# Performance work log

Measured on AMD Instinct MI355X. Metric: run time of the kernel, lower is better.

The kernel has to match this reference:

```python
import jax, jax.numpy as jnp
import numpy as np
from jax import lax

B, CIN, T = 16, 2, 4096
DM, DI, DS, DR, DC, NL = 128, 256, 16, 8, 4, 6  # d_model, d_inner, d_state, dt_rank, d_conv, n_layers


def setup_inputs():
    ks = iter(jax.random.split(jax.random.key(0), 48))
    def rn(shape, s=0.05):
        return jax.random.normal(next(ks), shape, jnp.float32) * s
    rng = np.random.default_rng(0)
    n_mask = int(round(0.25 / 0.02))
    starts = rng.choice(np.linspace(0.0, 1.0, int(round(1 / 0.02)), endpoint=False), n_mask, replace=False)
    m = np.ones((B, CIN, T), np.float32)
    for s0 in starts:
        m[:, :, int(T * s0):int(T * (s0 + 0.02))] = 0.0
    return {
        'x': jax.random.normal(next(ks), (B, CIN, T), jnp.float32),
        'mask': jnp.asarray(m),
        'enc_W0': rn((32, CIN, 3), 0.3), 'enc_b0': jnp.zeros(32), 'enc_g0': jnp.ones(32), 'enc_be0': jnp.zeros(32),
        'enc_W1': rn((64, 32, 3), 0.1), 'enc_b1': jnp.zeros(64), 'enc_g1': jnp.ones(64), 'enc_be1': jnp.zeros(64),
        'enc_W2': rn((128, 64, 3), 0.08), 'enc_b2': jnp.zeros(128), 'enc_g2': jnp.ones(128), 'enc_be2': jnp.zeros(128),
        'ln_g': jnp.ones((NL, DM)), 'ln_b': jnp.zeros((NL, DM)),
        'in_W': rn((NL, 2 * DI, DM)), 'conv_W': rn((NL, DI, DC), 0.3), 'conv_b': jnp.zeros((NL, DI)),
        'xp_W': rn((NL, DR + 2 * DS, DI)), 'dt_W': rn((NL, DI, DR), 0.2),
        'dt_b': jnp.full((NL, DI), -4.6, jnp.float32),  # softplus -> dt ~ 0.01
        'A_log': jnp.tile(jnp.log(jnp.arange(1, DS + 1, dtype=jnp.float32)), (NL, DI, 1)),
        'D_p': jnp.ones((NL, DI)), 'out_W': rn((NL, DM, DI)),
        'nf_g': jnp.ones(DM), 'nf_b': jnp.zeros(DM),
        'dec_W0': rn((128, 64, 3), 0.08), 'dec_b0': jnp.zeros(64), 'dec_g0': jnp.ones(64), 'dec_be0': jnp.zeros(64),
        'dec_W1': rn((64, 32, 3), 0.1), 'dec_b1': jnp.zeros(32), 'dec_g1': jnp.ones(32), 'dec_be1': jnp.zeros(32),
        'dec_W2': rn((32, CIN, 3), 0.1), 'dec_b2': jnp.zeros(CIN),
    }


def _conv(x, W, b, stride, pad):
    y = lax.conv_general_dilated(x, W, (stride,), [(pad, pad)], dimension_numbers=('NCH', 'OIH', 'NCH'))
    return y + b[None, :, None]


def _deconv(x, W, b, stride=2, pad=1, out_pad=1):
    # torch ConvTranspose1d weight (in, out, k) -> flipped conv with lhs dilation
    k = W.shape[-1]
    Wc = jnp.flip(W, -1).transpose(1, 0, 2)
    y = lax.conv_general_dilated(x, Wc, (1,), [(k - 1 - pad, k - 1 - pad + out_pad)],
                                 lhs_dilation=(stride,), dimension_numbers=('NCH', 'OIH', 'NCH'))
    return y + b[None, :, None]


def _gn1(x, g, b, eps=1e-5):  # GroupNorm(1, C) over (C, L)
    m = x.mean((1, 2), keepdims=True)
    v = ((x - m) ** 2).mean((1, 2), keepdims=True)
    return (x - m) * lax.rsqrt(v + eps) * g[None, :, None] + b[None, :, None]


def _ln(x, g, b, eps=1e-5):
    m = x.mean(-1, keepdims=True)
    v = ((x - m) ** 2).mean(-1, keepdims=True)
    return (x - m) * lax.rsqrt(v + eps) * g + b


def _mamba(u, in_W, conv_W, conv_b, xp_W, dt_W, dt_b, A_log, D_p, out_W):
    # u: (B, L, DM)
    xz = jnp.einsum('bld,ed->ble', u, in_W)            # (B, L, 2*DI)
    xi, z = xz[..., :DI], xz[..., DI:]
    xc = jnp.pad(xi.transpose(0, 2, 1), ((0, 0), (0, 0), (DC - 1, 0)))  # causal pad
    xc = lax.conv_general_dilated(xc, conv_W[:, None, :], (1,), [(0, 0)],
                                  feature_group_count=DI, dimension_numbers=('NCH', 'OIH', 'NCH'))
    xc = jax.nn.silu(xc + conv_b[None, :, None]).transpose(0, 2, 1)     # (B, L, DI)
    dbl = jnp.einsum('bld,ed->ble', xc, xp_W)          # (B, L, DR+2*DS)
    dt = jax.nn.softplus(jnp.einsum('blr,dr->bld', dbl[..., :DR], dt_W) + dt_b)
    Bm = dbl[..., DR:DR + DS]
    Cm = dbl[..., DR + DS:]
    A = -jnp.exp(A_log)                                # (DI, DS)
    dA = jnp.exp(dt[..., None] * A)                    # (B, L, DI, DS)
    dBx = dt[..., None] * Bm[:, :, None, :] * xc[..., None]
    def comb(e1, e2):
        a1, b1 = e1
        a2, b2 = e2
        return a1 * a2, a2 * b1 + b2
    _, h = lax.associative_scan(comb, (dA, dBx), axis=1)  # selective scan over L
    y = jnp.einsum('blds,bls->bld', h, Cm) + D_p * xc
    y = y * jax.nn.silu(z)
    return jnp.einsum('bld,ed->ble', y, out_W)          # (B, L, DM)


def _forward(x, mask, enc_W0, enc_b0, enc_g0, enc_be0, enc_W1, enc_b1, enc_g1, enc_be1,
             enc_W2, enc_b2, enc_g2, enc_be2, ln_g, ln_b, in_W, conv_W, conv_b, xp_W,
             dt_W, dt_b, A_log, D_p, out_W, nf_g, nf_b,
             dec_W0, dec_b0, dec_g0, dec_be0, dec_W1, dec_b1, dec_g1, dec_be1, dec_W2, dec_b2):
    gelu = lambda t: jax.nn.gelu(t, approximate=False)
    h = mask * x
    h = gelu(_gn1(_conv(h, enc_W0, enc_b0, 2, 1), enc_g0, enc_be0))
    h = gelu(_gn1(_conv(h, enc_W1, enc_b1, 2, 1), enc_g1, enc_be1))
    h = gelu(_gn1(_conv(h, enc_W2, enc_b2, 2, 1), enc_g2, enc_be2))
    s = h.transpose(0, 2, 1)                            # (B, L=T/8, DM)
    for i in range(NL):
        s = s + _mamba(_ln(s, ln_g[i], ln_b[i]), in_W[i], conv_W[i], conv_b[i],
                       xp_W[i], dt_W[i], dt_b[i], A_log[i], D_p[i], out_W[i])
    s = _ln(s, nf_g, nf_b)
    d = s.transpose(0, 2, 1)
    d = gelu(_gn1(_deconv(d, dec_W0, dec_b0), dec_g0, dec_be0))
    d = gelu(_gn1(_deconv(d, dec_W1, dec_b1), dec_g1, dec_be1))
    d = _deconv(d, dec_W2, dec_b2)                      # (B, CIN, T), no norm/act on last block
    return d


def reference(x, mask, enc_W0, enc_b0, enc_g0, enc_be0, enc_W1, enc_b1, enc_g1, enc_be1,
              enc_W2, enc_b2, enc_g2, enc_be2, ln_g, ln_b, in_W, conv_W, conv_b, xp_W,
              dt_W, dt_b, A_log, D_p, out_W, nf_g, nf_b,
              dec_W0, dec_b0, dec_g0, dec_be0, dec_W1, dec_b1, dec_g1, dec_be1, dec_W2, dec_b2):
    d = _forward(x, mask, enc_W0, enc_b0, enc_g0, enc_be0, enc_W1, enc_b1, enc_g1, enc_be1,
                 enc_W2, enc_b2, enc_g2, enc_be2, ln_g, ln_b, in_W, conv_W, conv_b, xp_W,
                 dt_W, dt_b, A_log, D_p, out_W, nf_g, nf_b,
                 dec_W0, dec_b0, dec_g0, dec_be0, dec_W1, dec_b1, dec_g1, dec_be1, dec_W2, dec_b2)
    return (d, x, mask)
```

## Files before the change

### kernel.cpp

```cpp
#include <hip/hip_runtime.h>
#include <hip/hip_bf16.h>
#include <math.h>

#define NB 16
#define TT 4096
#define LL 512
#define DM 128
#define DI 256
#define NLAYER 6
#define CL 32
#define NCH 16

typedef __bf16 bf16x8 __attribute__((ext_vector_type(8)));
typedef float f32x4 __attribute__((ext_vector_type(4)));
typedef unsigned short ushort;

static __device__ __forceinline__ float gelu_f(float v){
  return 0.5f*v*(1.f + erff(v*0.70710678118654752f));
}
static __device__ __forceinline__ float silu_f(float v){
  return v/(1.f + __expf(-v));
}
static __device__ __forceinline__ ushort f2b(float v){
  __hip_bfloat16 h = __float2bfloat16(v);
  return *(ushort*)&h;
}

__global__ __launch_bounds__(256) void k_maskmul(const float* __restrict__ x, const float* __restrict__ m,
                          float* __restrict__ out, int n){
  int i = blockIdx.x*256 + threadIdx.x;
  if (i < n) out[i] = x[i]*m[i];
}

__global__ __launch_bounds__(256) void k_castb(const float* __restrict__ in, ushort* __restrict__ out, int n){
  int i = blockIdx.x*256 + threadIdx.x;
  if (i < n) out[i] = f2b(in[i]);
}

__global__ __launch_bounds__(256) void k_trw(const float* __restrict__ in, float* __restrict__ out, int Ci, int Co){
  int idx = blockIdx.x*256 + threadIdx.x;
  int n = Ci*Co*3;
  if (idx >= n) return;
  int k = idx % 3;
  int o = (idx/3) % Co;
  int ci = idx/(3*Co);
  out[((size_t)o*Ci + ci)*3 + k] = in[idx];
}

template<int Ci, int Co, int TW, int OS>
__global__ __launch_bounds__(256) void k_conv_lds(const float* __restrict__ x, const float* __restrict__ W,
                        const float* __restrict__ bias, float* __restrict__ y, int Li){
  const int Lc = TW;
  const int Lo = Li >> 1;
  const int S  = Lo / Lc;
  const int CoB = Co / OS;
  __shared__ float xe[Ci][Lc+1];
  __shared__ float xo[Ci][Lc+1];
  int bid = blockIdx.x;
  int os = bid % OS;
  int ch = (bid / OS) % S;
  int b  = bid / (OS*S);
  int t0 = ch*Lc;
  const float* xb = x + (size_t)b*Ci*Li;
  for (int idx = threadIdx.x; idx < Ci*(2*Lc+1); idx += 256){
    int ci = idx / (2*Lc+1);
    int j  = idx - ci*(2*Lc+1);
    int gin = 2*t0 - 1 + j;
    float v = (gin >= 0 && gin < Li) ? xb[(size_t)ci*Li + gin] : 0.f;
    if (j & 1) xo[ci][j>>1] = v;
    else       xe[ci][j>>1] = v;
  }
  __syncthreads();
  const int NOg = 256/TW;
  const int OI  = CoB/NOg;
  int tl = threadIdx.x % TW;
  int og = threadIdx.x / TW;
  #pragma unroll
  for (int oi = 0; oi < OI; oi++){
    int o = os*CoB + oi*NOg + og;
    const float* w = W + (size_t)o*Ci*3;
    float acc = bias[o];
    #pragma unroll 4
    for (int ci = 0; ci < Ci; ci++){
      float w0 = w[ci*3+0], w1 = w[ci*3+1], w2 = w[ci*3+2];
      acc += w0*xe[ci][tl] + w1*xo[ci][tl] + w2*xe[ci][tl+1];
    }
    y[((size_t)b*Co + o)*Lo + t0 + tl] = acc;
  }
}

__global__ __launch_bounds__(256) void k_gn_part(const float* __restrict__ x, float* __restrict__ gp){
  int b = blockIdx.x >> 3, k8 = blockIdx.x & 7;
  const float* xb = x + (size_t)b*65536 + (size_t)k8*8192;
  float s = 0.f, s2 = 0.f;
  for (int i = threadIdx.x; i < 8192; i += 256){ float v = xb[i]; s += v; s2 += v*v; }
  #pragma unroll
  for (int o = 32; o; o >>= 1){ s += __shfl_down(s, o); s2 += __shfl_down(s2, o); }
  __shared__ float sh[8];
  int wid = threadIdx.x >> 6;
  if ((threadIdx.x & 63) == 0){ sh[wid] = s; sh[wid+4] = s2; }
  __syncthreads();
  if (threadIdx.x == 0){
    float a = sh[0]+sh[1]+sh[2]+sh[3], a2 = sh[4]+sh[5]+sh[6]+sh[7];
    gp[(b*8+k8)*2+0] = a; gp[(b*8+k8)*2+1] = a2;
  }
}
__global__ __launch_bounds__(256) void k_gn_apply(float* __restrict__ x, const float* __restrict__ g,
                          const float* __restrict__ be, int Tl, const float* __restrict__ gp){
  int gidx = blockIdx.x*256 + threadIdx.x;
  int b = gidx >> 16, i = gidx & 65535;
  float s = 0.f, s2 = 0.f;
  #pragma unroll
  for (int k = 0; k < 8; k++){ s += gp[(b*8+k)*2]; s2 += gp[(b*8+k)*2+1]; }
  float mean = s*(1.f/65536.f);
  float inv  = rsqrtf(s2*(1.f/65536.f) - mean*mean + 1e-5f);
  int c = i / Tl;
  float* p = x + (size_t)b*65536 + i;
  float v = (*p - mean)*inv*g[c] + be[c];
  *p = gelu_f(v);
}

__global__ __launch_bounds__(256) void k_transpose2(const float* __restrict__ in, float* __restrict__ out){
  int idx = blockIdx.x*256 + threadIdx.x;
  if (idx >= NB*DM*LL) return;
  int t = idx & 511;
  int c = (idx >> 9) & 127;
  int b = idx >> 16;
  out[(size_t)b*65536 + (size_t)t*128 + c] = in[idx];
}

__global__ __launch_bounds__(256) void k_transposeB(const float* __restrict__ in, float* __restrict__ out){
  int idx = blockIdx.x*256 + threadIdx.x;
  if (idx >= NB*DM*LL) return;
  int m = idx & 511;
  int c = (idx >> 9) & 127;
  int b = idx >> 16;
  out[idx] = in[(size_t)b*65536 + (size_t)m*128 + c];
}

__global__ __launch_bounds__(256) void k_ln2(const float* __restrict__ x, const float* __restrict__ g,
                      const float* __restrict__ be, float* __restrict__ out, int rows){
  int row = blockIdx.x*4 + (threadIdx.x >> 6);
  if (row >= rows) return;
  int lid = threadIdx.x & 63;
  const float* xr = x + (size_t)row*DM;
  float v0 = xr[lid], v1 = xr[lid+64];
  float s = v0 + v1;
  #pragma unroll
  for (int o = 32; o; o >>= 1) s += __shfl_xor(s, o);
  float mean = s*(1.f/128.f);
  float d0 = v0-mean, d1 = v1-mean;
  float s2 = d0*d0 + d1*d1;
  #pragma unroll
  for (int o = 32; o; o >>= 1) s2 += __shfl_xor(s2, o);
  float inv = rsqrtf(s2*(1.f/128.f) + 1e-5f);
  float* orow = out + (size_t)row*DM;
  orow[lid]    = d0*inv*g[lid]    + be[lid];
  orow[lid+64] = d1*inv*g[lid+64] + be[lid+64];
}

__global__ __launch_bounds__(256) void k_ln2b(const float* __restrict__ x, const float* __restrict__ g,
                      const float* __restrict__ be, ushort* __restrict__ out, int rows){
  int row = blockIdx.x*4 + (threadIdx.x >> 6);
  if (row >= rows) return;
  int lid = threadIdx.x & 63;
  const float* xr = x + (size_t)row*DM;
  float v0 = xr[lid], v1 = xr[lid+64];
  float s = v0 + v1;
  #pragma unroll
  for (int o = 32; o; o >>= 1) s += __shfl_xor(s, o);
  float mean = s*(1.f/128.f);
  float d0 = v0-mean, d1 = v1-mean;
  float s2 = d0*d0 + d1*d1;
  #pragma unroll
  for (int o = 32; o; o >>= 1) s2 += __shfl_xor(s2, o);
  float inv = rsqrtf(s2*(1.f/128.f) + 1e-5f);
  ushort* orow = out + (size_t)row*DM;
  orow[lid]    = f2b(d0*inv*g[lid]    + be[lid]);
  orow[lid+64] = f2b(d1*inv*g[lid+64] + be[lid+64]);
}

__global__ __launch_bounds__(256) void k_mfma_split(const ushort* __restrict__ A, const ushort* __restrict__ B,
                          float* __restrict__ C0, float* __restrict__ C1, int K){
  int tid = threadIdx.x;
  int wid = tid >> 6, l = tid & 63;
  int wm = wid >> 1, wn = wid & 1;
  int m0 = blockIdx.y*128 + wm*64;
  int n0 = blockIdx.x*128 + wn*64;
  int lr = l & 15;
  int lk = (l >> 4)*8;
  int orow = (l >> 4)*4;
  f32x4 acc[4][4];
  #pragma unroll
  for (int i = 0; i < 4; i++)
    #pragma unroll
    for (int j = 0; j < 4; j++) acc[i][j] = (f32x4){0.f,0.f,0.f,0.f};
  for (int k0 = 0; k0 < K; k0 += 32){
    bf16x8 a[4], b[4];
    #pragma unroll
    for (int f = 0; f < 4; f++)
      a[f] = *(const bf16x8*)(A + (size_t)(m0 + f*16 + lr)*K + k0 + lk);
    #pragma unroll
    for (int f = 0; f < 4; f++)
      b[f] = *(const bf16x8*)(B + (size_t)(n0 + f*16 + lr)*K + k0 + lk);
    #pragma unroll
    for (int i = 0; i < 4; i++)
      #pragma unroll
      for (int j = 0; j < 4; j++)
        acc[i][j] = __builtin_amdgcn_mfma_f32_16x16x32_bf16(a[i], b[j], acc[i][j], 0, 0, 0);
  }
  float* C    = (n0 < 256) ? C0 : C1;
  int ncol0   = (n0 < 256) ? n0 : n0 - 256;
  #pragma unroll
  for (int i = 0; i < 4; i++)
    #pragma unroll
    for (int j = 0; j < 4; j++)
      #pragma unroll
      for (int r = 0; r < 4; r++)
        C[(size_t)(m0 + i*16 + orow + r)*256 + ncol0 + j*16 + lr] = acc[i][j][r];
}

__global__ __launch_bounds__(256) void k_mfma_acc2(const ushort* __restrict__ A, const ushort* __restrict__ B,
                          float* __restrict__ C, int K){
  int tid = threadIdx.x;
  int wid = tid >> 6, l = tid & 63;
  int m0 = blockIdx.x*32;
  int n0 = wid*32;
  int lr = l & 15;
  int lk = (l >> 4)*8;
  int orow = (l >> 4)*4;
  f32x4 acc[2][2];
  #pragma unroll
  for (int i = 0; i < 2; i++)
    #pragma unroll
    for (int j = 0; j < 2; j++)
      #pragma unroll
      for (int r = 0; r < 4; r++)
        acc[i][j][r] = C[(size_t)(m0 + i*16 + orow + r)*128 + n0 + j*16 + lr];
  for (int k0 = 0; k0 < K; k0 += 32){
    bf16x8 a[2], b[2];
    #pragma unroll
    for (int f = 0; f < 2; f++)
      a[f] = *(const bf16x8*)(A + (size_t)(m0 + f*16 + lr)*K + k0 + lk);
    #pragma unroll
    for (int f = 0; f < 2; f++)
      b[f] = *(const bf16x8*)(B + (size_t)(n0 + f*16 + lr)*K + k0 + lk);
    #pragma unroll
    for (int i = 0; i < 2; i++)
      #pragma unroll
      for (int j = 0; j < 2; j++)
        acc[i][j] = __builtin_amdgcn_mfma_f32_16x16x32_bf16(a[i], b[j], acc[i][j], 0, 0, 0);
  }
  #pragma unroll
  for (int i = 0; i < 2; i++)
    #pragma unroll
    for (int j = 0; j < 2; j++)
      #pragma unroll
      for (int r = 0; r < 4; r++)
        C[(size_t)(m0 + i*16 + orow + r)*128 + n0 + j*16 + lr] = acc[i][j][r];
}

__global__ __launch_bounds__(256) void k_gemm_xp(const float* __restrict__ A, const float* __restrict__ B,
                          float* __restrict__ C){
  __shared__ float As[32][17];
  __shared__ float Bs[64][17];
  int tid = threadIdx.x;
  int m0 = blockIdx.x*32;
  int tx = tid & 15, ty = tid >> 4;
  float acc[2][4] = {};
  for (int k0 = 0; k0 < 256; k0 += 16){
    if (tid < 128){
      int r = tid >> 2, c = (tid & 3)*4;
      float4 av = *(const float4*)(A + (size_t)(m0+r)*256 + k0 + c);
      As[r][c]=av.x; As[r][c+1]=av.y; As[r][c+2]=av.z; As[r][c+3]=av.w;
    }
    {
      int r = tid >> 2, c = (tid & 3)*4;
      float4 bv = make_float4(0.f,0.f,0.f,0.f);
      if (r < 40) bv = *(const float4*)(B + (size_t)r*256 + k0 + c);
      Bs[r][c]=bv.x; Bs[r][c+1]=bv.y; Bs[r][c+2]=bv.z; Bs[r][c+3]=bv.w;
    }
    __syncthreads();
    #pragma unroll
    for (int k = 0; k < 16; k++){
      float a[2], bb[4];
      #pragma unroll
      for (int i = 0; i < 2; i++) a[i] = As[ty*2+i][k];
      #pragma unroll
      for (int j = 0; j < 4; j++) bb[j] = Bs[tx*4+j][k];
      #pragma unroll
      for (int i = 0; i < 2; i++)
        #pragma unroll
        for (int j = 0; j < 4; j++) acc[i][j] += a[i]*bb[j];
    }
    __syncthreads();
  }
  #pragma unroll
  for (int i = 0; i < 2; i++){
    int m = m0 + ty*2 + i;
    #pragma unroll
    for (int j = 0; j < 4; j++){
      int n = tx*4 + j;
      if (n < 40) C[(size_t)m*40 + n] = acc[i][j];
    }
  }
}

__global__ __launch_bounds__(256) void k_cconv2(const float* __restrict__ xi, const float* __restrict__ cw,
                         const float* __restrict__ cb, float* __restrict__ xc){
  int idx = blockIdx.x*256 + threadIdx.x;
  if (idx >= NB*LL*DI) return;
  int d = idx & 255;
  int l = (idx >> 8) & 511;
  int b = idx >> 17;
  const float* xp = xi + (size_t)b*131072 + d;
  float acc = cb[d];
  #pragma unroll
  for (int j = 0; j < 4; j++){
    int m = l - 3 + j;
    if (m >= 0) acc += xp[(size_t)m*256]*cw[d*4 + j];
  }
  xc[idx] = silu_f(acc);
}

__global__ __launch_bounds__(256) void k_scan_sum(const float* __restrict__ xc, const float* __restrict__ dbl,
                        const float* __restrict__ dtW, const float* __restrict__ dtb,
                        const float* __restrict__ Alog,
                        float* __restrict__ GA, float* __restrict__ GB){
  __shared__ float srow[CL*40];
  int bid = blockIdx.x;
  int b = bid >> 4, ch = bid & 15;
  int d = threadIdx.x;
  const float* dbp = dbl + (size_t)b*20480 + ch*CL*40;
  for (int j = d; j < CL*40; j += 256) srow[j] = dbp[j];
  float4 w0 = *(const float4*)(dtW + d*8);
  float4 w1 = *(const float4*)(dtW + d*8 + 4);
  float tb = dtb[d];
  float a[16];
  #pragma unroll
  for (int s = 0; s < 16; s++) a[s] = -__expf(Alog[d*16 + s]);
  const float* xcp = xc + (size_t)b*131072 + (size_t)ch*CL*256 + d;
  __syncthreads();
  float A[16], Bv[16];
  #pragma unroll
  for (int s = 0; s < 16; s++){ A[s] = 1.f; Bv[s] = 0.f; }
  #pragma unroll 2
  for (int i = 0; i < CL; i++){
    const float* r = srow + i*40;
    float raw = tb + r[0]*w0.x + r[1]*w0.y + r[2]*w0.z + r[3]*w0.w
                   + r[4]*w1.x + r[5]*w1.y + r[6]*w1.z + r[7]*w1.w;
    float dt = (raw > 20.f) ? raw : log1pf(__expf(raw));
    float xcv = xcp[(size_t)i*256];
    float dxc = dt*xcv;
    #pragma unroll
    for (int s = 0; s < 16; s++){
      float e = __expf(dt*a[s]);
      A[s] *= e;
      Bv[s] = e*Bv[s] + dxc*r[8+s];
    }
  }
  size_t base = (((size_t)b*NCH + ch)*16)*256 + d;
  #pragma unroll
  for (int s = 0; s < 16; s++){
    GA[base + (size_t)s*256] = A[s];
    GB[base + (size_t)s*256] = Bv[s];
  }
}

__global__ __launch_bounds__(256) void k_scan_pre(const float* __restrict__ GA, float* __restrict__ GB){
  int gid = blockIdx.x*256 + threadIdx.x;
  int b = gid >> 12;
  int s = (gid >> 8) & 15;
  int d = gid & 255;
  size_t stride = (size_t)16*256;
  size_t idx = (((size_t)b*NCH)*16 + s)*256 + d;
  float P = 0.f;
  #pragma unroll
  for (int ch = 0; ch < NCH; ch++){
    float Ac = GA[idx], Bc = GB[idx];
    GB[idx] = P;
    P = Ac*P + Bc;
    idx += stride;
  }
}

__global__ __launch_bounds__(256) void k_scan_emit(const float* __restrict__ xc, const float* __restrict__ dbl,
                        const float* __restrict__ z,
                        const float* __restrict__ dtW, const float* __restrict__ dtb,
                        const float* __restrict__ Alog, const float* __restrict__ Dp,
                        const float* __restrict__ GB, ushort* __restrict__ yb){
  __shared__ float srow[CL*40];
  int bid = blockIdx.x;
  int b = bid >> 4, ch = bid & 15;
  int d = threadIdx.x;
  const float* dbp = dbl + (size_t)b*20480 + ch*CL*40;
  for (int j = d; j < CL*40; j += 256) srow[j] = dbp[j];
  float4 w0 = *(const float4*)(dtW + d*8);
  float4 w1 = *(const float4*)(dtW + d*8 + 4);
  float tb = dtb[d];
  float Dd = Dp[d];
  float a[16];
  #pragma unroll
  for (int s = 0; s < 16; s++) a[s] = -__expf(Alog[d*16 + s]);
  float h[16];
  size_t base = (((size_t)b*NCH + ch)*16)*256 + d;
  #pragma unroll
  for (int s = 0; s < 16; s++) h[s] = GB[base + (size_t)s*256];
  const float* xcp = xc + (size_t)b*131072 + (size_t)ch*CL*256 + d;
  const float* zp  = z  + (size_t)b*131072 + (size_t)ch*CL*256 + d;
  ushort* yp = yb + (size_t)b*131072 + (size_t)ch*CL*256 + d;
  __syncthreads();
  #pragma unroll 2
  for (int i = 0; i < CL; i++){
    const float* r = srow + i*40;
    float raw = tb + r[0]*w0.x + r[1]*w0.y + r[2]*w0.z + r[3]*w0.w
                   + r[4]*w1.x + r[5]*w1.y + r[6]*w1.z + r[7]*w1.w;
    float dt = (raw > 20.f) ? raw : log1pf(__expf(raw));
    float xcv = xcp[(size_t)i*256];
    float dxc = dt*xcv;
    float y = Dd*xcv;
    #pragma unroll
    for (int s = 0; s < 16; s++){
      float e = __expf(dt*a[s]);
      h[s] = e*h[s] + dxc*r[8+s];
      y += h[s]*r[24+s];
    }
    float zv = zp[(size_t)i*256];
    yp[(size_t)i*256] = f2b(y*silu_f(zv));
  }
}

template<int Ci, int Co, int TW, int OS>
__global__ __launch_bounds__(256) void k_deconv_lds(const float* __restrict__ x, const float* __restrict__ WT,
                          const float* __restrict__ bias, float* __restrict__ y, int Li, int cs){
  const int Lc = TW;
  const int S  = Li / Lc;
  const int CoB = Co / OS;
  __shared__ float xin[Ci][Lc+1];
  int bid = blockIdx.x;
  int os = bid % OS;
  int ch = (bid / OS) % S;
  int b  = bid / (OS*S);
  int m0 = ch*Lc;
  const float* xb = x + (size_t)b*Ci*Li;
  for (int idx = threadIdx.x; idx < Ci*(Lc+1); idx += 256){
    int ci = idx / (Lc+1);
    int q  = idx - ci*(Lc+1);
    int m  = m0 + q;
    xin[ci][q] = (m < Li) ? xb[(size_t)ci*cs + m] : 0.f;
  }
  __syncthreads();
  const int NOg = 256/TW;
  const int OI  = CoB/NOg;
  int tl = threadIdx.x % TW;
  int og = threadIdx.x / TW;
  float* yo = y + (size_t)b*Co*(size_t)(2*Li);
  #pragma unroll
  for (int oi = 0; oi < OI; oi++){
    int o = os*CoB + oi*NOg + og;
    const float* w = WT + (size_t)o*Ci*3;
    float bo = bias[o];
    float even = bo, odd = bo;
    #pragma unroll 4
    for (int ci = 0; ci < Ci; ci++){
      float w0 = w[ci*3+0], w1 = w[ci*3+1], w2 = w[ci*3+2];
      float xm  = xin[ci][tl];
      float xm1 = xin[ci][tl+1];
      even += w1*xm;
      odd  += w2*xm + w0*xm1;
    }
    *(float2*)(yo + (size_t)o*(2*Li) + 2*(m0 + tl)) = make_float2(even, odd);
  }
}

__global__ __launch_bounds__(256) void k_deconv2p(const float* __restrict__ x, const float* __restrict__ W,
                          const float* __restrict__ bias, float* __restrict__ y,
                          int Ci, int Co, int Li, int cs, int S){
  __shared__ float w[384];
  int bid = blockIdx.x;
  int ch = bid % S;
  int o  = (bid / S) % Co;
  int b  = bid / (S*Co);
  for (int j = threadIdx.x; j < Ci*3; j += 256){
    int i = j/3, k = j - 3*i;
    w[j] = W[((size_t)i*Co + o)*3 + k];
  }
  __syncthreads();
  int Lc = Li / S;
  int m0 = ch*Lc;
  const float* xb = x + (size_t)b*Ci*Li;
  float bo = bias[o];
  float* yo = y + ((size_t)b*Co + o)*(size_t)(2*Li);
  for (int idx = threadIdx.x; idx < Lc; idx += 256){
    int m = m0 + idx;
    float even = bo, odd = bo;
    bool has1 = (m + 1 < Li);
    for (int i = 0; i < Ci; i++){
      const float* xr = xb + (size_t)i*cs;
      float xm  = xr[m];
      float xm1 = has1 ? xr[m+1] : 0.f;
      even += w[i*3+1]*xm;
      odd  += w[i*3+2]*xm + w[i*3+0]*xm1;
    }
    *(float2*)(yo + 2*m) = make_float2(even, odd);
  }
}

__global__ __launch_bounds__(256) void k_copyf(const float* __restrict__ in, float* __restrict__ out, int n){
  int i = blockIdx.x*256 + threadIdx.x;
  if (i < n) out[i] = in[i];
}

extern "C" void kernel_launch(void* const* d_in, const int* in_sizes, int n_in,
                              void* d_out, int out_size, void* d_ws, size_t ws_size,
                              hipStream_t stream) {
  const float* x      = (const float*)d_in[0];
  const float* mask   = (const float*)d_in[1];
  const float* enc_W0 = (const float*)d_in[2];
  const float* enc_b0 = (const float*)d_in[3];
  const float* enc_g0 = (const float*)d_in[4];
  const float* enc_be0= (const float*)d_in[5];
  const float* enc_W1 = (const float*)d_in[6];
  const float* enc_b1 = (const float*)d_in[7];
  const float* enc_g1 = (const float*)d_in[8];
  const float* enc_be1= (const float*)d_in[9];
  const float* enc_W2 = (const float*)d_in[10];
  const float* enc_b2 = (const float*)d_in[11];
  const float* enc_g2 = (const float*)d_in[12];
  const float* enc_be2= (const float*)d_in[13];
  const float* ln_g   = (const float*)d_in[14];
  const float* ln_b   = (const float*)d_in[15];
  const float* in_W   = (const float*)d_in[16];
  const float* conv_W = (const float*)d_in[17];
  const float* conv_b = (const float*)d_in[18];
  const float* xp_W   = (const float*)d_in[19];
  const float* dt_W   = (const float*)d_in[20];
  const float* dt_b   = (const float*)d_in[21];
  const float* A_log  = (const float*)d_in[22];
  const float* D_p    = (const float*)d_in[23];
  const float* out_W  = (const float*)d_in[24];
  const float* nf_g   = (const float*)d_in[25];
  const float* nf_b   = (const float*)d_in[26];
  const float* dec_W0 = (const float*)d_in[27];
  const float* dec_b0 = (const float*)d_in[28];
  const float* dec_g0 = (const float*)d_in[29];
  const float* dec_be0= (const float*)d_in[30];
  const float* dec_W1 = (const float*)d_in[31];
  const float* dec_b1 = (const float*)d_in[32];
  const float* dec_g1 = (const float*)d_in[33];
  const float* dec_be1= (const float*)d_in[34];
  const float* dec_W2 = (const float*)d_in[35];
  const float* dec_b2 = (const float*)d_in[36];

  float* out = (float*)d_out;

  float* ws  = (float*)d_ws;
  float* S    = ws;
  float* U    = S    + 1048576;
  float* XI   = U    + 1048576;
  float* Z    = XI   + 2097152;
  float* CBUF = Z    + 2097152;
  float* GA   = CBUF + 2097152;
  float* GB   = GA   + 1048576;
  float* DBL  = GB   + 1048576;
  float* WBIN = DBL  + 327680;
  float* WBOUT= WBIN + 196608;
  float* WT0  = WBOUT+ 98304;
  float* WT1  = WT0  + 24576;
  float* EB0 = XI;
  float* EB1 = XI + 1048576;
  float* H0  = CBUF;
  float* UT  = CBUF;
  float* GNP = DBL;
  ushort* Ub    = (ushort*)U;
  ushort* Yb    = (ushort*)GA;
  ushort* WbIn  = (ushort*)WBIN;
  ushort* WbOut = (ushort*)WBOUT;

  k_castb<<<1536, 256, 0, stream>>>(in_W,  WbIn,  NLAYER*512*DM);
  k_castb<<<768, 256, 0, stream>>>(out_W, WbOut, NLAYER*DM*DI);
  k_trw<<<96, 256, 0, stream>>>(dec_W0, WT0, 128, 64);
  k_trw<<<24, 256, 0, stream>>>(dec_W1, WT1, 64, 32);

  k_maskmul<<<512, 256, 0, stream>>>(x, mask, H0, NB*2*TT);
  k_conv_lds<2,32,64,1><<<512, 256, 0, stream>>>(H0, enc_W0, enc_b0, EB0, 4096);
  k_gn_part<<<128, 256, 0, stream>>>(EB0, GNP);
  k_gn_apply<<<4096, 256, 0, stream>>>(EB0, enc_g0, enc_be0, 2048, GNP);
  k_conv_lds<32,64,32,2><<<1024, 256, 0, stream>>>(EB0, enc_W1, enc_b1, EB1, 2048);
  k_gn_part<<<128, 256, 0, stream>>>(EB1, GNP);
  k_gn_apply<<<4096, 256, 0, stream>>>(EB1, enc_g1, enc_be1, 1024, GNP);
  k_conv_lds<64,128,32,4><<<1024, 256, 0, stream>>>(EB1, enc_W2, enc_b2, EB0, 1024);
  k_gn_part<<<128, 256, 0, stream>>>(EB0, GNP);
  k_gn_apply<<<4096, 256, 0, stream>>>(EB0, enc_g2, enc_be2, 512, GNP);
  k_transpose2<<<4096, 256, 0, stream>>>(EB0, S);

  const int rows = NB*LL;
  for (int i = 0; i < NLAYER; i++){
    k_ln2b<<<2048, 256, 0, stream>>>(S, ln_g + i*DM, ln_b + i*DM, Ub, rows);
    k_mfma_split<<<dim3(4, 64), 256, 0, stream>>>(Ub, WbIn + (size_t)i*512*DM, XI, Z, DM);
    k_cconv2<<<8192, 256, 0, stream>>>(XI, conv_W + (size_t)i*DI*4, conv_b + (size_t)i*DI, CBUF);
    k_gemm_xp<<<256, 256, 0, stream>>>(CBUF, xp_W + (size_t)i*40*DI, DBL);
    k_scan_sum<<<256, 256, 0, stream>>>(CBUF, DBL,
                                        dt_W + (size_t)i*DI*8, dt_b + (size_t)i*DI,
                                        A_log + (size_t)i*DI*16, GA, GB);
    k_scan_pre<<<256, 256, 0, stream>>>(GA, GB);
    k_scan_emit<<<256, 256, 0, stream>>>(CBUF, DBL, Z,
                                         dt_W + (size_t)i*DI*8, dt_b + (size_t)i*DI,
                                         A_log + (size_t)i*DI*16, D_p + (size_t)i*DI, GB, Yb);
    k_mfma_acc2<<<256, 256, 0, stream>>>(Yb, WbOut + (size_t)i*DM*DI, S, DI);
  }

  k_ln2<<<2048, 256, 0, stream>>>(S, nf_g, nf_b, U, rows);
  k_transposeB<<<4096, 256, 0, stream>>>(U, UT);
  k_deconv_lds<128,64,16,2><<<1024, 256, 0, stream>>>(UT, WT0, dec_b0, EB0, 512, 512);
  k_gn_part<<<128, 256, 0, stream>>>(EB0, GNP);
  k_gn_apply<<<4096, 256, 0, stream>>>(EB0, dec_g0, dec_be0, 1024, GNP);
  k_deconv_lds<64,32,32,2><<<1024, 256, 0, stream>>>(EB0, WT1, dec_b1, EB1, 1024, 1024);
  k_gn_part<<<128, 256, 0, stream>>>(EB1, GNP);
  k_gn_apply<<<4096, 256, 0, stream>>>(EB1, dec_g1, dec_be1, 2048, GNP);
  k_deconv2p<<<16*2*8, 256, 0, stream>>>(EB1, dec_W2, dec_b2, out, 32, 2, 2048, 2048, 8);

  k_copyf<<<512, 256, 0, stream>>>(x,    out + 131072, 131072);
  k_copyf<<<512, 256, 0, stream>>>(mask, out + 262144, 131072);
}
```

Before: 801.7 us.

## Fuse causal conv into x_proj GEMM and fold chunk prefix into scan emit

```diff
diff --git a/kernel.cpp b/kernel.cpp
--- a/kernel.cpp
+++ b/kernel.cpp
@@ -260,19 +260,37 @@
         C[(size_t)(m0 + i*16 + orow + r)*128 + n0 + j*16 + lr] = acc[i][j][r];
 }
 
-__global__ __launch_bounds__(256) void k_gemm_xp(const float* __restrict__ A, const float* __restrict__ B,
-                          float* __restrict__ C){
+__global__ __launch_bounds__(256) void k_gemm_xp_f(const float* __restrict__ xi, const float* __restrict__ cw,
+                          const float* __restrict__ cb, const float* __restrict__ B,
+                          float* __restrict__ xc, float* __restrict__ C){
   __shared__ float As[32][17];
   __shared__ float Bs[64][17];
   int tid = threadIdx.x;
   int m0 = blockIdx.x*32;
+  int b  = blockIdx.x >> 4;
+  int l0 = (blockIdx.x & 15)*32;
+  const float* xb = xi + (size_t)b*131072;
   int tx = tid & 15, ty = tid >> 4;
   float acc[2][4] = {};
   for (int k0 = 0; k0 < 256; k0 += 16){
     if (tid < 128){
       int r = tid >> 2, c = (tid & 3)*4;
-      float4 av = *(const float4*)(A + (size_t)(m0+r)*256 + k0 + c);
-      As[r][c]=av.x; As[r][c+1]=av.y; As[r][c+2]=av.z; As[r][c+3]=av.w;
+      int l = l0 + r;
+      float4 res;
+      float rv[4];
+      #pragma unroll
+      for (int jj = 0; jj < 4; jj++){
+        int d = k0 + c + jj;
+        float4 w4 = *(const float4*)(cw + d*4);
+        float a = cb[d] + xb[(size_t)l*256 + d]*w4.w;
+        if (l >= 1) a += xb[(size_t)(l-1)*256 + d]*w4.z;
+        if (l >= 2) a += xb[(size_t)(l-2)*256 + d]*w4.y;
+        if (l >= 3) a += xb[(size_t)(l-3)*256 + d]*w4.x;
+        rv[jj] = silu_f(a);
+        As[r][c+jj] = rv[jj];
+      }
+      res = make_float4(rv[0], rv[1], rv[2], rv[3]);
+      *(float4*)(xc + (size_t)b*131072 + (size_t)l*256 + k0 + c) = res;
     }
     {
       int r = tid >> 2, c = (tid & 3)*4;
@@ -304,23 +322,6 @@
       if (n < 40) C[(size_t)m*40 + n] = acc[i][j];
     }
   }
-}
-
-__global__ __launch_bounds__(256) void k_cconv2(const float* __restrict__ xi, const float* __restrict__ cw,
-                         const float* __restrict__ cb, float* __restrict__ xc){
-  int idx = blockIdx.x*256 + threadIdx.x;
-  if (idx >= NB*LL*DI) return;
-  int d = idx & 255;
-  int l = (idx >> 8) & 511;
-  int b = idx >> 17;
-  const float* xp = xi + (size_t)b*131072 + d;
-  float acc = cb[d];
-  #pragma unroll
-  for (int j = 0; j < 4; j++){
-    int m = l - 3 + j;
-    if (m >= 0) acc += xp[(size_t)m*256]*cw[d*4 + j];
-  }
-  xc[idx] = silu_f(acc);
 }
 
 __global__ __launch_bounds__(256) void k_scan_sum(const float* __restrict__ xc, const float* __restrict__ dbl,
@@ -367,28 +368,12 @@
   }
 }
 
-__global__ __launch_bounds__(256) void k_scan_pre(const float* __restrict__ GA, float* __restrict__ GB){
-  int gid = blockIdx.x*256 + threadIdx.x;
-  int b = gid >> 12;
-  int s = (gid >> 8) & 15;
-  int d = gid & 255;
-  size_t stride = (size_t)16*256;
-  size_t idx = (((size_t)b*NCH)*16 + s)*256 + d;
-  float P = 0.f;
-  #pragma unroll
-  for (int ch = 0; ch < NCH; ch++){
-    float Ac = GA[idx], Bc = GB[idx];
-    GB[idx] = P;
-    P = Ac*P + Bc;
-    idx += stride;
-  }
-}
-
 __global__ __launch_bounds__(256) void k_scan_emit(const float* __restrict__ xc, const float* __restrict__ dbl,
                         const float* __restrict__ z,
                         const float* __restrict__ dtW, const float* __restrict__ dtb,
                         const float* __restrict__ Alog, const float* __restrict__ Dp,
-                        const float* __restrict__ GB, ushort* __restrict__ yb){
+                        const float* __restrict__ GA, const float* __restrict__ GBr,
+                        ushort* __restrict__ yb){
   __shared__ float srow[CL*40];
   int bid = blockIdx.x;
   int b = bid >> 4, ch = bid & 15;
@@ -403,9 +388,21 @@
   #pragma unroll
   for (int s = 0; s < 16; s++) a[s] = -__expf(Alog[d*16 + s]);
   float h[16];
-  size_t base = (((size_t)b*NCH + ch)*16)*256 + d;
-  #pragma unroll
-  for (int s = 0; s < 16; s++) h[s] = GB[base + (size_t)s*256];
+  #pragma unroll
+  for (int s = 0; s < 16; s++) h[s] = 0.f;
+  {
+    size_t cstride = (size_t)16*256;
+    size_t bb = (((size_t)b*NCH)*16)*256 + d;
+    for (int cc = 0; cc < ch; cc++){
+      #pragma unroll
+      for (int s = 0; s < 16; s++){
+        float Ac = GA[bb + (size_t)s*256];
+        float Bc = GBr[bb + (size_t)s*256];
+        h[s] = Ac*h[s] + Bc;
+      }
+      bb += cstride;
+    }
+  }
   const float* xcp = xc + (size_t)b*131072 + (size_t)ch*CL*256 + d;
   const float* zp  = z  + (size_t)b*131072 + (size_t)ch*CL*256 + d;
   ushort* yp = yb + (size_t)b*131072 + (size_t)ch*CL*256 + d;
@@ -598,15 +595,14 @@
   for (int i = 0; i < NLAYER; i++){
     k_ln2b<<<2048, 256, 0, stream>>>(S, ln_g + i*DM, ln_b + i*DM, Ub, rows);
     k_mfma_split<<<dim3(4, 64), 256, 0, stream>>>(Ub, WbIn + (size_t)i*512*DM, XI, Z, DM);
-    k_cconv2<<<8192, 256, 0, stream>>>(XI, conv_W + (size_t)i*DI*4, conv_b + (size_t)i*DI, CBUF);
-    k_gemm_xp<<<256, 256, 0, stream>>>(CBUF, xp_W + (size_t)i*40*DI, DBL);
+    k_gemm_xp_f<<<256, 256, 0, stream>>>(XI, conv_W + (size_t)i*DI*4, conv_b + (size_t)i*DI,
+                                         xp_W + (size_t)i*40*DI, CBUF, DBL);
     k_scan_sum<<<256, 256, 0, stream>>>(CBUF, DBL,
                                         dt_W + (size_t)i*DI*8, dt_b + (size_t)i*DI,
                                         A_log + (size_t)i*DI*16, GA, GB);
-    k_scan_pre<<<256, 256, 0, stream>>>(GA, GB);
     k_scan_emit<<<256, 256, 0, stream>>>(CBUF, DBL, Z,
                                          dt_W + (size_t)i*DI*8, dt_b + (size_t)i*DI,
-                                         A_log + (size_t)i*DI*16, D_p + (size_t)i*DI, GB, Yb);
+                                         A_log + (size_t)i*DI*16, D_p + (size_t)i*DI, GA, GB, Yb);
     k_mfma_acc2<<<256, 256, 0, stream>>>(Yb, WbOut + (size_t)i*DM*DI, S, DI);
   }
 
```

After: 1.038 ms. 29.5% more time.
